# Kernel tuning notes

Measured on AMD Instinct MI355X. Metric: run time of the kernel, lower is better.

The kernel has to match this reference:

```python
import jax, jax.numpy as jnp
import numpy as np

Z_DIM = 3
H = 128
N_BLOCKS = 4
N = 30000
E = 180000
T = 2


def _mlp2(x, W1, b1, W2, b2):
    return jnp.maximum(x @ W1 + b1, 0.0) @ W2 + b2


def _stats(x, eps=1e-8):
    # batch mean/std as accumulated by the running-stat Normalizer (buffers -> no grad)
    m = x.mean(0)
    v = jnp.maximum((x * x).mean(0) - m * m, 0.0)
    s = jnp.maximum(jnp.sqrt(v), eps)
    return jax.lax.stop_gradient(m), jax.lax.stop_gradient(s)


def setup_inputs() -> dict:
    key = jax.random.key(0)
    ks = jax.random.split(key, 32)

    def w(k, shape, fan_in):
        return jax.random.normal(k, shape, jnp.float32) / np.sqrt(fan_in).astype(np.float32)

    inp = {}
    inp["z"] = jax.random.normal(ks[0], (T, N, Z_DIM), jnp.float32)
    inp["z_target"] = jax.random.normal(ks[1], (N, Z_DIM), jnp.float32)
    inp["pos"] = jax.random.uniform(ks[2], (N, 2), jnp.float32)
    # encoder node MLP: z_dim -> H -> H
    inp["enc_node_W1"] = w(ks[3], (Z_DIM, H), Z_DIM)
    inp["enc_node_b1"] = jnp.zeros((H,), jnp.float32)
    inp["enc_node_W2"] = w(ks[4], (H, H), H)
    inp["enc_node_b2"] = jnp.zeros((H,), jnp.float32)
    # encoder edge MLP: edge_dim(3) -> H -> H
    inp["enc_edge_W1"] = w(ks[5], (3, H), 3)
    inp["enc_edge_b1"] = jnp.zeros((H,), jnp.float32)
    inp["enc_edge_W2"] = w(ks[6], (H, H), H)
    inp["enc_edge_b2"] = jnp.zeros((H,), jnp.float32)
    # decoder MLP: H -> H -> z_dim
    inp["dec_W1"] = w(ks[7], (H, H), H)
    inp["dec_b1"] = jnp.zeros((H,), jnp.float32)
    inp["dec_W2"] = w(ks[8], (H, Z_DIM), H)
    inp["dec_b2"] = jnp.zeros((Z_DIM,), jnp.float32)
    # GraphNetBlocks, stacked over n_blocks
    inp["blk_edge_W1"] = w(ks[9], (N_BLOCKS, 3 * H, H), 3 * H)
    inp["blk_edge_b1"] = jnp.zeros((N_BLOCKS, H), jnp.float32)
    inp["blk_edge_W2"] = w(ks[10], (N_BLOCKS, H, H), H)
    inp["blk_edge_b2"] = jnp.zeros((N_BLOCKS, H), jnp.float32)
    inp["blk_node_W1"] = w(ks[11], (N_BLOCKS, 2 * H, H), 2 * H)
    inp["blk_node_b1"] = jnp.zeros((N_BLOCKS, H), jnp.float32)
    inp["blk_node_W2"] = w(ks[12], (N_BLOCKS, H, H), H)
    inp["blk_node_b2"] = jnp.zeros((N_BLOCKS, H), jnp.float32)
    # bidirectional mesh edges (triangles_to_edges output)
    inp["senders"] = jax.random.randint(ks[13], (E,), 0, N, jnp.int64)
    inp["receivers"] = jax.random.randint(ks[14], (E,), 0, N, jnp.int64)
    return inp


def reference(z, z_target, pos,
              enc_node_W1, enc_node_b1, enc_node_W2, enc_node_b2,
              enc_edge_W1, enc_edge_b1, enc_edge_W2, enc_edge_b2,
              dec_W1, dec_b1, dec_W2, dec_b2,
              blk_edge_W1, blk_edge_b1, blk_edge_W2, blk_edge_b2,
              blk_node_W1, blk_node_b1, blk_node_W2, blk_node_b2,
              senders, receivers):
    zl = z[-1]                                   # [N, z_dim]
    n_nodes = zl.shape[0]

    # --- build_graph ---
    rel = pos[senders] - pos[receivers]          # [E, 2]
    ef_raw = jnp.concatenate([rel, jnp.linalg.norm(rel, axis=1, keepdims=True)], axis=1)  # [E, 3]
    em, es = _stats(ef_raw)
    ef = _mlp2((ef_raw - em) / es, enc_edge_W1, enc_edge_b1, enc_edge_W2, enc_edge_b2)    # [E, H]
    nm, ns = _stats(zl)
    nf = _mlp2((zl - nm) / ns, enc_node_W1, enc_node_b1, enc_node_W2, enc_node_b2)        # [N, H]

    # --- message passing blocks ---
    def block(carry, p):
        nf, ef = carry
        eW1, eb1, eW2, eb2, nW1, nb1, nW2, nb2 = p
        e_in = jnp.concatenate([ef, nf[senders], nf[receivers]], axis=1)   # [E, 3H]
        ef = _mlp2(e_in, eW1, eb1, eW2, eb2) + ef
        agg = jax.ops.segment_sum(ef, receivers, num_segments=n_nodes)    # [N, H]
        n_in = jnp.concatenate([nf, agg], axis=1)                          # [N, 2H]
        nf = _mlp2(n_in, nW1, nb1, nW2, nb2) + nf
        return (nf, ef), None

    (nf, ef), _ = jax.lax.scan(block, (nf, ef),
                               (blk_edge_W1, blk_edge_b1, blk_edge_W2, blk_edge_b2,
                                blk_node_W1, blk_node_b1, blk_node_W2, blk_node_b2))

    # --- decode + loss ---
    output = _mlp2(nf, dec_W1, dec_b1, dec_W2, dec_b2)                     # [N, z_dim]
    target = z_target - zl
    om, os = _stats(target)
    target_normalized = (target - om) / os
    loss = jnp.mean((target_normalized - output) ** 2)

    z_update = jax.lax.stop_gradient(output) * os + om                     # Normalizer.inverse(detach)
    z_pred = zl + z_update
    rmse = jnp.mean(jnp.sqrt(jnp.mean((z_pred - z_target) ** 2, axis=0)))
    return z_pred, loss, rmse
```

## Files before the change

### kernel.cpp

```cpp
#include <hip/hip_runtime.h>
#include <hip/hip_bf16.h>
#include <math.h>

#define HDIM 128
#define TPB 256

typedef __attribute__((ext_vector_type(8))) short bf16x8;
typedef __attribute__((ext_vector_type(4))) float f32x4;

static inline int ceil_div(int a, int b){ return (a + b - 1) / b; }

__device__ __forceinline__ float wave_sum(float v){
#pragma unroll
  for (int o = 32; o > 0; o >>= 1) v += __shfl_down(v, o, 64);
  return v;
}

__device__ __forceinline__ short f2bf(float f){
  __hip_bfloat16 h = __float2bfloat16(f);
  return *reinterpret_cast<short*>(&h);
}
__device__ __forceinline__ float bfb2f(short s){
  unsigned int u = ((unsigned int)(unsigned short)s) << 16;
  return __builtin_bit_cast(float, u);
}

__device__ __forceinline__ void gl_lds16(const short* g, short* l){
  __builtin_amdgcn_global_load_lds(
      (const __attribute__((address_space(1))) void*)g,
      (__attribute__((address_space(3))) void*)l, 16, 0, 0);
}

__global__ void edge_raw_stats(const float* __restrict__ pos,
                               const int* __restrict__ snd,
                               const int* __restrict__ rcv,
                               float* __restrict__ ef_raw,
                               float* __restrict__ epart, int E){
  __shared__ float red[4][6];
  int tid = threadIdx.x, w = tid >> 6, l = tid & 63;
  int e = blockIdx.x * blockDim.x + tid;
  float s[6] = {0.f,0.f,0.f,0.f,0.f,0.f};
  if (e < E){
    int si = snd[e], ri = rcv[e];
    float rx = pos[2*si]   - pos[2*ri];
    float ry = pos[2*si+1] - pos[2*ri+1];
    float nm = sqrtf(rx*rx + ry*ry);
    ef_raw[3*e]   = rx;
    ef_raw[3*e+1] = ry;
    ef_raw[3*e+2] = nm;
    s[0] = rx; s[1] = ry; s[2] = nm;
    s[3] = rx*rx; s[4] = ry*ry; s[5] = nm*nm;
  }
#pragma unroll
  for (int k = 0; k < 6; k++) s[k] = wave_sum(s[k]);
  if (l == 0)
#pragma unroll
    for (int k = 0; k < 6; k++) red[w][k] = s[k];
  __syncthreads();
  if (tid < 6)
    epart[(size_t)blockIdx.x * 6 + tid] =
      red[0][tid] + red[1][tid] + red[2][tid] + red[3][tid];
}

__global__ void node_stats(const float* __restrict__ zl,
                           const float* __restrict__ z_target,
                           float* __restrict__ npart, int N){
  __shared__ float red[4][12];
  int tid = threadIdx.x, w = tid >> 6, l = tid & 63;
  int n = blockIdx.x * blockDim.x + tid;
  float s[12];
#pragma unroll
  for (int i = 0; i < 12; i++) s[i] = 0.f;
  if (n < N){
#pragma unroll
    for (int d = 0; d < 3; d++){
      float z = zl[3*n+d];
      float t = z_target[3*n+d] - z;
      s[d]   = z;  s[3+d] = z*z;
      s[6+d] = t;  s[9+d] = t*t;
    }
  }
#pragma unroll
  for (int i = 0; i < 12; i++) s[i] = wave_sum(s[i]);
  if (l == 0)
#pragma unroll
    for (int i = 0; i < 12; i++) red[w][i] = s[i];
  __syncthreads();
  if (tid < 12)
    npart[(size_t)blockIdx.x * 12 + tid] =
      red[0][tid] + red[1][tid] + red[2][tid] + red[3][tid];
}

__global__ void reduce_stats(const float* __restrict__ ep, int ne,
                             const float* __restrict__ np_, int nn,
                             float* __restrict__ raw){
  __shared__ float red[4];
  int tid = threadIdx.x, w = tid >> 6, l = tid & 63;
  for (int j = 0; j < 6; j++){
    float s = 0.f;
    for (int b = tid; b < ne; b += 256) s += ep[(size_t)b * 6 + j];
    s = wave_sum(s);
    if (l == 0) red[w] = s;
    __syncthreads();
    if (tid == 0) raw[j] = red[0] + red[1] + red[2] + red[3];
    __syncthreads();
  }
  for (int j = 0; j < 12; j++){
    float s = 0.f;
    for (int b = tid; b < nn; b += 256) s += np_[(size_t)b * 12 + j];
    s = wave_sum(s);
    if (l == 0) red[w] = s;
    __syncthreads();
    if (tid == 0) raw[6 + j] = red[0] + red[1] + red[2] + red[3];
    __syncthreads();
  }
}

__global__ void finalize_stats(const float* __restrict__ raw,
                               float* __restrict__ fin, int E, int N){
#pragma unroll
  for (int d = 0; d < 3; d++){
    float cE = (float)E, cN = (float)N;
    float m, v;
    m = raw[0+d] / cE; v = fmaxf(raw[3+d]/cE - m*m, 0.f);
    fin[0+d] = m;  fin[3+d]  = fmaxf(sqrtf(v), 1e-8f);
    m = raw[6+d] / cN; v = fmaxf(raw[9+d]/cN - m*m, 0.f);
    fin[6+d] = m;  fin[9+d]  = fmaxf(sqrtf(v), 1e-8f);
    m = raw[12+d] / cN; v = fmaxf(raw[15+d]/cN - m*m, 0.f);
    fin[12+d] = m; fin[15+d] = fmaxf(sqrtf(v), 1e-8f);
  }
}

__global__ void csr_hist(const int* __restrict__ rcv, int* __restrict__ deg, int E){
  int e = blockIdx.x * blockDim.x + threadIdx.x;
  if (e < E) atomicAdd(&deg[rcv[e]], 1);
}

__global__ void csr_scan(const int* __restrict__ deg, int* __restrict__ row_start,
                         int N, int E){
  __shared__ int part[1024];
  int t = threadIdx.x;
  int chunk = (N + 1023) / 1024;
  int lo = t * chunk, hi = min(lo + chunk, N);
  int s = 0;
  for (int i = lo; i < hi; i++) s += deg[i];
  part[t] = s;
  __syncthreads();
  for (int off = 1; off < 1024; off <<= 1){
    int v = (t >= off) ? part[t - off] : 0;
    __syncthreads();
    part[t] += v;
    __syncthreads();
  }
  int base = (t == 0) ? 0 : part[t - 1];
  for (int i = lo; i < hi; i++){
    row_start[i] = base;
    base += deg[i];
  }
  if (t == 1023) row_start[N] = E;
}

__global__ void csr_scatter(const int* __restrict__ rcv, int* __restrict__ cursor,
                            int* __restrict__ eids, int E){
  int e = blockIdx.x * blockDim.x + threadIdx.x;
  if (e < E){
    int p = atomicAdd(&cursor[rcv[e]], 1);
    eids[p] = e;
  }
}

__global__ void pack_weights(const float* __restrict__ encEW2,
                             const float* __restrict__ encNW2,
                             const float* __restrict__ decW1,
                             const float* __restrict__ beW1,
                             const float* __restrict__ beW2,
                             const float* __restrict__ bnW1,
                             const float* __restrict__ bnW2,
                             __hip_bfloat16* __restrict__ wp){
  int y = blockIdx.y;
  const float* src; __hip_bfloat16* dst; int K;
  if (y == 0){ src = encEW2; dst = wp;          K = 128; }
  else if (y == 1){ src = encNW2; dst = wp + 16384; K = 128; }
  else if (y == 2){ src = decW1;  dst = wp + 32768; K = 128; }
  else {
    int b = (y - 3) >> 2, j = (y - 3) & 3;
    __hip_bfloat16* base = wp + 49152 + b * 114688;
    if (j == 0){ src = beW1 + b*49152; dst = base;          K = 384; }
    else if (j == 1){ src = beW2 + b*16384; dst = base + 49152; K = 128; }
    else if (j == 2){ src = bnW1 + b*32768; dst = base + 65536; K = 256; }
    else { src = bnW2 + b*16384; dst = base + 98304; K = 128; }
  }
  int id = blockIdx.x * blockDim.x + threadIdx.x;
  if (id >= 128 * K) return;
  int c = id >> 12;
  int r = id & 4095;
  int t = r >> 9;
  int l = (r >> 3) & 63;
  int j = r & 7;
  int k = c * 32 + ((l >> 4) << 3) + j;
  int n = t * 16 + (l & 15);
  dst[id] = __float2bfloat16(src[k * 128 + n]);
}

__launch_bounds__(256)
__global__ void encoder_fused(const float* __restrict__ raw,
                              const float* __restrict__ mptr,
                              const float* __restrict__ sptr,
                              const float* __restrict__ W1,
                              const float* __restrict__ b1,
                              const __hip_bfloat16* __restrict__ W2f,
                              const float* __restrict__ b2,
                              __hip_bfloat16* __restrict__ out, int rows){
  __shared__ __align__(16) short bsh[16384];
  const int tid = threadIdx.x, w = tid >> 6, l = tid & 63, m = l & 15, q = l >> 4;
  const short* wsrc = (const short*)W2f;
#pragma unroll
  for (int i = 0; i < 8; i++){
    int inst = w * 8 + i;
    gl_lds16(wsrc + inst * 512 + l * 8, &bsh[inst * 512]);
  }

  float s0 = mptr[0], s1 = mptr[1], s2 = mptr[2];
  float d0 = sptr[0], d1 = sptr[1], d2 = sptr[2];
  const int row0 = blockIdx.x * 64 + w * 16;
  const int ra = min(row0 + m, rows - 1);
  float x0 = (raw[3*ra]   - s0) / d0;
  float x1 = (raw[3*ra+1] - s1) / d1;
  float x2 = (raw[3*ra+2] - s2) / d2;
  bf16x8 afr[4];
#pragma unroll
  for (int c = 0; c < 4; c++){
    int nb = c * 32 + q * 8;
#pragma unroll
    for (int j = 0; j < 8; j++){
      float h = b1[nb+j] + x0 * W1[nb+j] + x1 * W1[128+nb+j] + x2 * W1[256+nb+j];
      afr[c][j] = f2bf(fmaxf(h, 0.f));
    }
  }
  f32x4 acc[8];
#pragma unroll
  for (int t = 0; t < 8; t++) acc[t] = (f32x4){0.f,0.f,0.f,0.f};
  __syncthreads();
#pragma unroll
  for (int c = 0; c < 4; c++){
#pragma unroll
    for (int t = 0; t < 8; t++){
      bf16x8 b = *(const bf16x8*)&bsh[(c*8 + t)*512 + l*8];
      acc[t] = __builtin_amdgcn_mfma_f32_16x16x32_bf16(afr[c], b, acc[t], 0, 0, 0);
    }
  }
  const int row_d = row0 + q * 4;
#pragma unroll
  for (int t = 0; t < 8; t++){
    int col = t * 16 + m;
    float bb = b2[col];
#pragma unroll
    for (int r = 0; r < 4; r++){
      int e = row_d + r;
      if (e < rows) out[(size_t)e * HDIM + col] = __float2bfloat16(acc[t][r] + bb);
    }
  }
}

__launch_bounds__(256)
__global__ void gemm128_g(const __hip_bfloat16* __restrict__ A,
                          const __hip_bfloat16* __restrict__ Wf,
                          const float* __restrict__ bias,
                          float* __restrict__ out, int rows){
  __shared__ __align__(16) short bsh[16384];
  const int tid = threadIdx.x, w = tid >> 6, l = tid & 63, m = l & 15, q = l >> 4;
  const short* wsrc = (const short*)Wf;
#pragma unroll
  for (int i = 0; i < 8; i++){
    int inst = w * 8 + i;
    gl_lds16(wsrc + inst * 512 + l * 8, &bsh[inst * 512]);
  }
  const int row0 = blockIdx.x * 64 + w * 16;
  const int ra = min(row0 + m, rows - 1);
  const short* pa = (const short*)A + (size_t)ra * HDIM + q * 8;
  bf16x8 afr[4];
#pragma unroll
  for (int c = 0; c < 4; c++) afr[c] = *(const bf16x8*)(pa + c * 32);
  f32x4 acc[8];
#pragma unroll
  for (int t = 0; t < 8; t++) acc[t] = (f32x4){0.f,0.f,0.f,0.f};
  __syncthreads();
#pragma unroll
  for (int c = 0; c < 4; c++){
#pragma unroll
    for (int t = 0; t < 8; t++){
      bf16x8 b = *(const bf16x8*)&bsh[(c*8 + t)*512 + l*8];
      acc[t] = __builtin_amdgcn_mfma_f32_16x16x32_bf16(afr[c], b, acc[t], 0, 0, 0);
    }
  }
  const int row_d = row0 + q * 4;
#pragma unroll
  for (int t = 0; t < 8; t++){
    int col = t * 16 + m;
    float bb = bias[col];
#pragma unroll
    for (int r = 0; r < 4; r++){
      int e = row_d + r;
      if (e < rows) out[(size_t)e * HDIM + col] = fmaxf(acc[t][r] + bb, 0.f);
    }
  }
}

__launch_bounds__(256)
__global__ void edge_block(const int* __restrict__ snd,
                           const int* __restrict__ rcv,
                           const __hip_bfloat16* __restrict__ nf,
                           __hip_bfloat16* __restrict__ ef,
                           const __hip_bfloat16* __restrict__ Wfrag,
                           const float* __restrict__ b1,
                           const float* __restrict__ b2,
                           int E){
  __shared__ __align__(16) short bsh[2][4096];
  __shared__ __align__(16) short hsh[4][16][136];
  const int tid = threadIdx.x, w = tid >> 6, l = tid & 63, m = l & 15, q = l >> 4;
  const short* wsrc = (const short*)Wfrag;
  gl_lds16(wsrc + (w*2+0)*512 + l*8, &bsh[0][(w*2+0)*512]);
  gl_lds16(wsrc + (w*2+1)*512 + l*8, &bsh[0][(w*2+1)*512]);

  const int row0 = blockIdx.x * 64 + w * 16;
  const int ra = min(row0 + m, E - 1);
  const int si = snd[ra], ri = rcv[ra];
  const short* pe = (const short*)ef + (size_t)ra * HDIM + q * 8;
  const short* ps = (const short*)nf + (size_t)si * HDIM + q * 8;
  const short* pr = (const short*)nf + (size_t)ri * HDIM + q * 8;
  bf16x8 afr[12];
#pragma unroll
  for (int c = 0; c < 4; c++){
    afr[c]   = *(const bf16x8*)(pe + c * 32);
    afr[4+c] = *(const bf16x8*)(ps + c * 32);
    afr[8+c] = *(const bf16x8*)(pr + c * 32);
  }
  f32x4 acc[8];
#pragma unroll
  for (int t = 0; t < 8; t++) acc[t] = (f32x4){0.f,0.f,0.f,0.f};
  __syncthreads();
#pragma unroll
  for (int c = 0; c < 12; c++){
    {
      const short* src = wsrc + (c + 1) * 4096;
      short* dstb = &bsh[(c + 1) & 1][0];
      gl_lds16(src + (w*2+0)*512 + l*8, dstb + (w*2+0)*512);
      gl_lds16(src + (w*2+1)*512 + l*8, dstb + (w*2+1)*512);
    }
    const short* bb = &bsh[c & 1][0];
#pragma unroll
    for (int t = 0; t < 8; t++){
      bf16x8 b = *(const bf16x8*)(bb + t*512 + l*8);
      acc[t] = __builtin_amdgcn_mfma_f32_16x16x32_bf16(afr[c], b, acc[t], 0, 0, 0);
    }
    __syncthreads();
  }
#pragma unroll
  for (int t = 0; t < 8; t++){
    float bb = b1[t * 16 + m];
#pragma unroll
    for (int r = 0; r < 4; r++)
      hsh[w][q*4 + r][t*16 + m] = f2bf(fmaxf(acc[t][r] + bb, 0.f));
  }
  const short* ph = &hsh[w][m][0] + q * 8;
  f32x4 acc2[8];
#pragma unroll
  for (int t = 0; t < 8; t++) acc2[t] = (f32x4){0.f,0.f,0.f,0.f};
#pragma unroll
  for (int c = 12; c < 16; c++){
    if (c + 1 < 16){
      const short* src = wsrc + (c + 1) * 4096;
      short* dstb = &bsh[(c + 1) & 1][0];
      gl_lds16(src + (w*2+0)*512 + l*8, dstb + (w*2+0)*512);
      gl_lds16(src + (w*2+1)*512 + l*8, dstb + (w*2+1)*512);
    }
    bf16x8 a = *(const bf16x8*)(ph + (c - 12) * 32);
    const short* bb = &bsh[c & 1][0];
#pragma unroll
    for (int t = 0; t < 8; t++){
      bf16x8 b = *(const bf16x8*)(bb + t*512 + l*8);
      acc2[t] = __builtin_amdgcn_mfma_f32_16x16x32_bf16(a, b, acc2[t], 0, 0, 0);
    }
    if (c < 15) __syncthreads();
  }
#pragma unroll
  for (int t = 0; t < 8; t++){
    float bb = b2[t * 16 + m];
#pragma unroll
    for (int r = 0; r < 4; r++)
      hsh[w][q*4 + r][t*16 + m] = f2bf(acc2[t][r] + bb);
  }
  int orow = row0 + (l >> 2);
  if (orow < E){
    const short* src = &hsh[w][l >> 2][(l & 3) * 32];
    short* dst = (short*)ef + (size_t)orow * HDIM + (l & 3) * 32;
#pragma unroll
    for (int k = 0; k < 4; k++){
      bf16x8 vnew = *(const bf16x8*)(src + k * 8);
      bf16x8 vold = *(const bf16x8*)(dst + k * 8);
      bf16x8 vo;
#pragma unroll
      for (int j = 0; j < 8; j++) vo[j] = f2bf(bfb2f(vnew[j]) + bfb2f(vold[j]));
      *(bf16x8*)(dst + k * 8) = vo;
    }
  }
}

__launch_bounds__(256)
__global__ void node_block(const int* __restrict__ row_start,
                           const int* __restrict__ eids,
                           const __hip_bfloat16* __restrict__ ef,
                           __hip_bfloat16* __restrict__ nf,
                           const __hip_bfloat16* __restrict__ Wfrag,
                           const float* __restrict__ b1,
                           const float* __restrict__ b2,
                           int N){
  __shared__ __align__(16) short bsh[2][4096];
  __shared__ __align__(16) short hsh[4][16][136];
  const int tid = threadIdx.x, w = tid >> 6, l = tid & 63, m = l & 15, q = l >> 4;
  const short* wsrc = (const short*)Wfrag;
  gl_lds16(wsrc + (w*2+0)*512 + l*8, &bsh[0][(w*2+0)*512]);
  gl_lds16(wsrc + (w*2+1)*512 + l*8, &bsh[0][(w*2+1)*512]);

  const int row0 = blockIdx.x * 64 + w * 16;
  const int ra = min(row0 + m, N - 1);
  const short* pn = (const short*)nf + (size_t)ra * HDIM + q * 8;
  bf16x8 afr[8];
#pragma unroll
  for (int c = 0; c < 4; c++) afr[c] = *(const bf16x8*)(pn + c * 32);
  float sum[4][8];
#pragma unroll
  for (int c = 0; c < 4; c++)
#pragma unroll
    for (int j = 0; j < 8; j++) sum[c][j] = 0.f;
  int s0 = row_start[ra], s1 = row_start[ra + 1];
  for (int it = s0; it < s1; it++){
    int eid = eids[it];
    const short* pf = (const short*)ef + (size_t)eid * HDIM + q * 8;
#pragma unroll
    for (int c = 0; c < 4; c++){
      bf16x8 v = *(const bf16x8*)(pf + c * 32);
#pragma unroll
      for (int j = 0; j < 8; j++) sum[c][j] += bfb2f(v[j]);
    }
  }
#pragma unroll
  for (int c = 0; c < 4; c++)
#pragma unroll
    for (int j = 0; j < 8; j++) afr[4 + c][j] = f2bf(sum[c][j]);

  f32x4 acc[8];
#pragma unroll
  for (int t = 0; t < 8; t++) acc[t] = (f32x4){0.f,0.f,0.f,0.f};
  __syncthreads();
#pragma unroll
  for (int c = 0; c < 8; c++){
    {
      const short* src = wsrc + (c + 1) * 4096;
      short* dstb = &bsh[(c + 1) & 1][0];
      gl_lds16(src + (w*2+0)*512 + l*8, dstb + (w*2+0)*512);
      gl_lds16(src + (w*2+1)*512 + l*8, dstb + (w*2+1)*512);
    }
    const short* bb = &bsh[c & 1][0];
#pragma unroll
    for (int t = 0; t < 8; t++){
      bf16x8 b = *(const bf16x8*)(bb + t*512 + l*8);
      acc[t] = __builtin_amdgcn_mfma_f32_16x16x32_bf16(afr[c], b, acc[t], 0, 0, 0);
    }
    __syncthreads();
  }
#pragma unroll
  for (int t = 0; t < 8; t++){
    float bb = b1[t * 16 + m];
#pragma unroll
    for (int r = 0; r < 4; r++)
      hsh[w][q*4 + r][t*16 + m] = f2bf(fmaxf(acc[t][r] + bb, 0.f));
  }
  const short* ph = &hsh[w][m][0] + q * 8;
  f32x4 acc2[8];
#pragma unroll
  for (int t = 0; t < 8; t++) acc2[t] = (f32x4){0.f,0.f,0.f,0.f};
#pragma unroll
  for (int c = 8; c < 12; c++){
    if (c + 1 < 12){
      const short* src = wsrc + (c + 1) * 4096;
      short* dstb = &bsh[(c + 1) & 1][0];
      gl_lds16(src + (w*2+0)*512 + l*8, dstb + (w*2+0)*512);
      gl_lds16(src + (w*2+1)*512 + l*8, dstb + (w*2+1)*512);
    }
    bf16x8 a = *(const bf16x8*)(ph + (c - 8) * 32);
    const short* bb = &bsh[c & 1][0];
#pragma unroll
    for (int t = 0; t < 8; t++){
      bf16x8 b = *(const bf16x8*)(bb + t*512 + l*8);
      acc2[t] = __builtin_amdgcn_mfma_f32_16x16x32_bf16(a, b, acc2[t], 0, 0, 0);
    }
    if (c < 11) __syncthreads();
  }
#pragma unroll
  for (int t = 0; t < 8; t++){
    float bb = b2[t * 16 + m];
#pragma unroll
    for (int r = 0; r < 4; r++)
      hsh[w][q*4 + r][t*16 + m] = f2bf(acc2[t][r] + bb);
  }
  int orow = row0 + (l >> 2);
  if (orow < N){
    const short* src = &hsh[w][l >> 2][(l & 3) * 32];
    short* dst = (short*)nf + (size_t)orow * HDIM + (l & 3) * 32;
#pragma unroll
    for (int k = 0; k < 4; k++){
      bf16x8 vnew = *(const bf16x8*)(src + k * 8);
      bf16x8 vold = *(const bf16x8*)(dst + k * 8);
      bf16x8 vo;
#pragma unroll
      for (int j = 0; j < 8; j++) vo[j] = f2bf(bfb2f(vnew[j]) + bfb2f(vold[j]));
      *(bf16x8*)(dst + k * 8) = vo;
    }
  }
}

__global__ void dec_final(const float* __restrict__ hbuf,
                          const float* __restrict__ W2,
                          const float* __restrict__ b2,
                          float* __restrict__ outd, int rows){
  __shared__ float hl[64 * 129];
  __shared__ float Wl[HDIM * 3];
  __shared__ float bl[3];
  int t = threadIdx.x;
  int node0 = blockIdx.x * 64;
  for (int i = t; i < HDIM * 3; i += 256) Wl[i] = W2[i];
  if (t < 3) bl[t] = b2[t];
#pragma unroll
  for (int i = 0; i < 32; i++){
    int lin = t + i * 256;
    int r = lin >> 7;
    int c = lin & 127;
    int node = node0 + r;
    hl[r * 129 + c] = (node < rows) ? hbuf[(size_t)node * HDIM + c] : 0.f;
  }
  __syncthreads();
  if (t < 64){
    int node = node0 + t;
    if (node < rows){
      float a0 = bl[0], a1 = bl[1], a2 = bl[2];
      for (int k = 0; k < HDIM; k++){
        float v = hl[t * 129 + k];
        a0 += v * Wl[k * 3];
        a1 += v * Wl[k * 3 + 1];
        a2 += v * Wl[k * 3 + 2];
      }
      outd[3 * node]     = a0;
      outd[3 * node + 1] = a1;
      outd[3 * node + 2] = a2;
    }
  }
}

__global__ void epilogue(const float* __restrict__ dec_out,
                         const float* __restrict__ zl,
                         const float* __restrict__ z_target,
                         const float* __restrict__ fin,
                         float* __restrict__ d_out,
                         float* __restrict__ lpart, int N){
  __shared__ float red[4][4];
  int tid = threadIdx.x, w = tid >> 6, l = tid & 63;
  int n = blockIdx.x * blockDim.x + tid;
  float s[4] = {0.f,0.f,0.f,0.f};
  if (n < N){
#pragma unroll
    for (int d = 0; d < 3; d++){
      float om = fin[12 + d], os = fin[15 + d];
      float o   = dec_out[3*n + d];
      float zld = zl[3*n + d];
      float zt  = z_target[3*n + d];
      float tgt = zt - zld;
      float tn  = (tgt - om) / os;
      float diff = tn - o;
      s[0] += diff * diff;
      float zp = zld + o * os + om;
      d_out[3*n + d] = zp;
      float e = zp - zt;
      s[1 + d] = e * e;
    }
  }
#pragma unroll
  for (int k = 0; k < 4; k++) s[k] = wave_sum(s[k]);
  if (l == 0)
#pragma unroll
    for (int k = 0; k < 4; k++) red[w][k] = s[k];
  __syncthreads();
  if (tid < 4)
    lpart[(size_t)blockIdx.x * 4 + tid] =
      red[0][tid] + red[1][tid] + red[2][tid] + red[3][tid];
}

__global__ void finalize_out(const float* __restrict__ lpart, int nb,
                             float* __restrict__ d_out, int N){
  __shared__ float red[4];
  __shared__ float vals[4];
  int tid = threadIdx.x, w = tid >> 6, l = tid & 63;
  for (int j = 0; j < 4; j++){
    float s = 0.f;
    for (int b = tid; b < nb; b += 256) s += lpart[(size_t)b * 4 + j];
    s = wave_sum(s);
    if (l == 0) red[w] = s;
    __syncthreads();
    if (tid == 0) vals[j] = red[0] + red[1] + red[2] + red[3];
    __syncthreads();
  }
  if (tid == 0){
    float cN = (float)N;
    float loss = vals[0] / (3.f * cN);
    float rmse = (sqrtf(vals[1] / cN) + sqrtf(vals[2] / cN) + sqrtf(vals[3] / cN)) / 3.f;
    d_out[(size_t)3 * N]     = loss;
    d_out[(size_t)3 * N + 1] = rmse;
  }
}

extern "C" void kernel_launch(void* const* d_in, const int* in_sizes, int n_in,
                              void* d_out, int out_size, void* d_ws, size_t ws_size,
                              hipStream_t stream){
  const float* z           = (const float*)d_in[0];
  const float* z_target    = (const float*)d_in[1];
  const float* pos         = (const float*)d_in[2];
  const float* enc_node_W1 = (const float*)d_in[3];
  const float* enc_node_b1 = (const float*)d_in[4];
  const float* enc_node_W2 = (const float*)d_in[5];
  const float* enc_node_b2 = (const float*)d_in[6];
  const float* enc_edge_W1 = (const float*)d_in[7];
  const float* enc_edge_b1 = (const float*)d_in[8];
  const float* enc_edge_W2 = (const float*)d_in[9];
  const float* enc_edge_b2 = (const float*)d_in[10];
  const float* dec_W1      = (const float*)d_in[11];
  const float* dec_b1      = (const float*)d_in[12];
  const float* dec_W2      = (const float*)d_in[13];
  const float* dec_b2      = (const float*)d_in[14];
  const float* blk_edge_W1 = (const float*)d_in[15];
  const float* blk_edge_b1 = (const float*)d_in[16];
  const float* blk_edge_W2 = (const float*)d_in[17];
  const float* blk_edge_b2 = (const float*)d_in[18];
  const float* blk_node_W1 = (const float*)d_in[19];
  const float* blk_node_b1 = (const float*)d_in[20];
  const float* blk_node_W2 = (const float*)d_in[21];
  const float* blk_node_b2 = (const float*)d_in[22];
  const int*   senders     = (const int*)d_in[23];
  const int*   receivers   = (const int*)d_in[24];

  const int N = in_sizes[1] / 3;
  const int E = in_sizes[23];
  const float* zl = z + (size_t)N * 3;

  const int neb = ceil_div(E, TPB);
  const int nnb = ceil_div(N, TPB);

  char* p = (char*)d_ws;
  auto carve = [&](size_t bytes) -> char* {
    char* r = p; p += (bytes + 255) & ~(size_t)255; return r;
  };
  float* stats_raw = (float*)carve(32 * 4);
  float* stats_fin = (float*)carve(32 * 4);
  float* epart     = (float*)carve((size_t)neb * 6 * 4);
  float* npart     = (float*)carve((size_t)nnb * 12 * 4);
  float* lpart     = (float*)carve((size_t)nnb * 4 * 4);
  float* ef_raw    = (float*)carve((size_t)E * 3 * 4);
  float* dec_out   = (float*)carve((size_t)N * 3 * 4);
  float* hbuf      = (float*)carve((size_t)N * HDIM * 4);
  int*   deg       = (int*)carve((size_t)N * 4);
  int*   row_start = (int*)carve((size_t)(N + 1) * 4);
  int*   cursor    = (int*)carve((size_t)N * 4);
  int*   eids      = (int*)carve((size_t)E * 4);
  __hip_bfloat16* wp = (__hip_bfloat16*)carve((size_t)507904 * 2);
  __hip_bfloat16* ef = (__hip_bfloat16*)carve((size_t)E * HDIM * 2);
  __hip_bfloat16* nf = (__hip_bfloat16*)carve((size_t)N * HDIM * 2);

  float* out = (float*)d_out;

  hipMemsetAsync(deg, 0, (size_t)N * 4, stream);

  edge_raw_stats<<<neb, TPB, 0, stream>>>(pos, senders, receivers, ef_raw, epart, E);
  node_stats<<<nnb, TPB, 0, stream>>>(zl, z_target, npart, N);
  reduce_stats<<<1, TPB, 0, stream>>>(epart, neb, npart, nnb, stats_raw);
  finalize_stats<<<1, 1, 0, stream>>>(stats_raw, stats_fin, E, N);

  csr_hist<<<neb, TPB, 0, stream>>>(receivers, deg, E);
  csr_scan<<<1, 1024, 0, stream>>>(deg, row_start, N, E);
  hipMemcpyAsync(cursor, row_start, (size_t)N * 4, hipMemcpyDeviceToDevice, stream);
  csr_scatter<<<neb, TPB, 0, stream>>>(receivers, cursor, eids, E);

  pack_weights<<<dim3(192, 19), TPB, 0, stream>>>(enc_edge_W2, enc_node_W2, dec_W1,
                                                  blk_edge_W1, blk_edge_W2,
                                                  blk_node_W1, blk_node_W2, wp);

  encoder_fused<<<ceil_div(E, 64), TPB, 0, stream>>>(ef_raw, stats_fin + 0, stats_fin + 3,
                                                     enc_edge_W1, enc_edge_b1,
                                                     wp, enc_edge_b2, ef, E);
  encoder_fused<<<ceil_div(N, 64), TPB, 0, stream>>>(zl, stats_fin + 6, stats_fin + 9,
                                                     enc_node_W1, enc_node_b1,
                                                     wp + 16384, enc_node_b2, nf, N);

  for (int b = 0; b < 4; b++){
    const __hip_bfloat16* eWf = wp + 49152 + (size_t)b * 114688;
    const __hip_bfloat16* nWf = eWf + 65536;
    const float* eb1 = blk_edge_b1 + (size_t)b * 128;
    const float* eb2 = blk_edge_b2 + (size_t)b * 128;
    const float* nb1 = blk_node_b1 + (size_t)b * 128;
    const float* nb2 = blk_node_b2 + (size_t)b * 128;

    edge_block<<<ceil_div(E, 64), TPB, 0, stream>>>(senders, receivers, nf, ef,
                                                    eWf, eb1, eb2, E);
    node_block<<<ceil_div(N, 64), TPB, 0, stream>>>(row_start, eids, ef, nf,
                                                    nWf, nb1, nb2, N);
  }

  gemm128_g<<<ceil_div(N, 64), TPB, 0, stream>>>(nf, wp + 32768, dec_b1, hbuf, N);
  dec_final<<<ceil_div(N, 64), TPB, 0, stream>>>(hbuf, dec_W2, dec_b2, dec_out, N);

  epilogue<<<nnb, TPB, 0, stream>>>(dec_out, zl, z_target, stats_fin,
                                    out, lpart, N);
  finalize_out<<<1, TPB, 0, stream>>>(lpart, nnb, out, N);
}
```

Baseline: 602.7 us.

## Store edges in receiver-sorted order and use 512-thread blocks for GNN blocks

Builds the CSR before the edge encoder and permutes edge features into receiver-sorted order, so the node aggregation reads contiguous edge rows instead of going through an eids indirection. The edge and receiver gathers in the edge kernel also become more local because edges sharing a receiver sit next to each other. Separately, edge_block and node_block now run 8 waves over 128 rows per block, so each wave loads one weight fragment per stage instead of two. This adds sorted sender and receiver arrays and doubles the LDS used for hidden staging.

```diff
diff --git a/kernel.cpp b/kernel.cpp
--- a/kernel.cpp
+++ b/kernel.cpp
@@ -31,9 +31,55 @@
       (__attribute__((address_space(3))) void*)l, 16, 0, 0);
 }
 
+__global__ void csr_hist(const int* __restrict__ rcv, int* __restrict__ deg, int E){
+  int e = blockIdx.x * blockDim.x + threadIdx.x;
+  if (e < E) atomicAdd(&deg[rcv[e]], 1);
+}
+
+__global__ void csr_scan(const int* __restrict__ deg, int* __restrict__ row_start,
+                         int N, int E){
+  __shared__ int part[1024];
+  int t = threadIdx.x;
+  int chunk = (N + 1023) / 1024;
+  int lo = t * chunk, hi = min(lo + chunk, N);
+  int s = 0;
+  for (int i = lo; i < hi; i++) s += deg[i];
+  part[t] = s;
+  __syncthreads();
+  for (int off = 1; off < 1024; off <<= 1){
+    int v = (t >= off) ? part[t - off] : 0;
+    __syncthreads();
+    part[t] += v;
+    __syncthreads();
+  }
+  int base = (t == 0) ? 0 : part[t - 1];
+  for (int i = lo; i < hi; i++){
+    row_start[i] = base;
+    base += deg[i];
+  }
+  if (t == 1023) row_start[N] = E;
+}
+
+__global__ void csr_scatter(const int* __restrict__ snd,
+                            const int* __restrict__ rcv,
+                            int* __restrict__ cursor,
+                            int* __restrict__ pinv,
+                            int* __restrict__ psnd,
+                            int* __restrict__ prcv, int E){
+  int e = blockIdx.x * blockDim.x + threadIdx.x;
+  if (e < E){
+    int r = rcv[e];
+    int p = atomicAdd(&cursor[r], 1);
+    pinv[e] = p;
+    psnd[p] = snd[e];
+    prcv[p] = r;
+  }
+}
+
 __global__ void edge_raw_stats(const float* __restrict__ pos,
                                const int* __restrict__ snd,
                                const int* __restrict__ rcv,
+                               const int* __restrict__ pinv,
                                float* __restrict__ ef_raw,
                                float* __restrict__ epart, int E){
   __shared__ float red[4][6];
@@ -45,9 +91,10 @@
     float rx = pos[2*si]   - pos[2*ri];
     float ry = pos[2*si+1] - pos[2*ri+1];
     float nm = sqrtf(rx*rx + ry*ry);
-    ef_raw[3*e]   = rx;
-    ef_raw[3*e+1] = ry;
-    ef_raw[3*e+2] = nm;
+    int p = pinv[e];
+    ef_raw[3*p]   = rx;
+    ef_raw[3*p+1] = ry;
+    ef_raw[3*p+2] = nm;
     s[0] = rx; s[1] = ry; s[2] = nm;
     s[3] = rx*rx; s[4] = ry*ry; s[5] = nm*nm;
   }
@@ -128,44 +175,6 @@
     fin[6+d] = m;  fin[9+d]  = fmaxf(sqrtf(v), 1e-8f);
     m = raw[12+d] / cN; v = fmaxf(raw[15+d]/cN - m*m, 0.f);
     fin[12+d] = m; fin[15+d] = fmaxf(sqrtf(v), 1e-8f);
-  }
-}
-
-__global__ void csr_hist(const int* __restrict__ rcv, int* __restrict__ deg, int E){
-  int e = blockIdx.x * blockDim.x + threadIdx.x;
-  if (e < E) atomicAdd(&deg[rcv[e]], 1);
-}
-
-__global__ void csr_scan(const int* __restrict__ deg, int* __restrict__ row_start,
-                         int N, int E){
-  __shared__ int part[1024];
-  int t = threadIdx.x;
-  int chunk = (N + 1023) / 1024;
-  int lo = t * chunk, hi = min(lo + chunk, N);
-  int s = 0;
-  for (int i = lo; i < hi; i++) s += deg[i];
-  part[t] = s;
-  __syncthreads();
-  for (int off = 1; off < 1024; off <<= 1){
-    int v = (t >= off) ? part[t - off] : 0;
-    __syncthreads();
-    part[t] += v;
-    __syncthreads();
-  }
-  int base = (t == 0) ? 0 : part[t - 1];
-  for (int i = lo; i < hi; i++){
-    row_start[i] = base;
-    base += deg[i];
-  }
-  if (t == 1023) row_start[N] = E;
-}
-
-__global__ void csr_scatter(const int* __restrict__ rcv, int* __restrict__ cursor,
-                            int* __restrict__ eids, int E){
-  int e = blockIdx.x * blockDim.x + threadIdx.x;
-  if (e < E){
-    int p = atomicAdd(&cursor[rcv[e]], 1);
-    eids[p] = e;
   }
 }
 
@@ -219,7 +228,6 @@
     int inst = w * 8 + i;
     gl_lds16(wsrc + inst * 512 + l * 8, &bsh[inst * 512]);
   }
-
   float s0 = mptr[0], s1 = mptr[1], s2 = mptr[2];
   float d0 = sptr[0], d1 = sptr[1], d2 = sptr[2];
   const int row0 = blockIdx.x * 64 + w * 16;
@@ -306,9 +314,9 @@
   }
 }
 
-__launch_bounds__(256)
-__global__ void edge_block(const int* __restrict__ snd,
-                           const int* __restrict__ rcv,
+__launch_bounds__(512)
+__global__ void edge_block(const int* __restrict__ psnd,
+                           const int* __restrict__ prcv,
                            const __hip_bfloat16* __restrict__ nf,
                            __hip_bfloat16* __restrict__ ef,
                            const __hip_bfloat16* __restrict__ Wfrag,
@@ -316,15 +324,14 @@
                            const float* __restrict__ b2,
                            int E){
   __shared__ __align__(16) short bsh[2][4096];
-  __shared__ __align__(16) short hsh[4][16][136];
+  __shared__ __align__(16) short hsh[8][16][136];
   const int tid = threadIdx.x, w = tid >> 6, l = tid & 63, m = l & 15, q = l >> 4;
   const short* wsrc = (const short*)Wfrag;
-  gl_lds16(wsrc + (w*2+0)*512 + l*8, &bsh[0][(w*2+0)*512]);
-  gl_lds16(wsrc + (w*2+1)*512 + l*8, &bsh[0][(w*2+1)*512]);
-
-  const int row0 = blockIdx.x * 64 + w * 16;
+  gl_lds16(wsrc + w*512 + l*8, &bsh[0][w*512]);
+
+  const int row0 = blockIdx.x * 128 + w * 16;
   const int ra = min(row0 + m, E - 1);
-  const int si = snd[ra], ri = rcv[ra];
+  const int si = psnd[ra], ri = prcv[ra];
   const short* pe = (const short*)ef + (size_t)ra * HDIM + q * 8;
   const short* ps = (const short*)nf + (size_t)si * HDIM + q * 8;
   const short* pr = (const short*)nf + (size_t)ri * HDIM + q * 8;
@@ -341,12 +348,7 @@
   __syncthreads();
 #pragma unroll
   for (int c = 0; c < 12; c++){
-    {
-      const short* src = wsrc + (c + 1) * 4096;
-      short* dstb = &bsh[(c + 1) & 1][0];
-      gl_lds16(src + (w*2+0)*512 + l*8, dstb + (w*2+0)*512);
-      gl_lds16(src + (w*2+1)*512 + l*8, dstb + (w*2+1)*512);
-    }
+    gl_lds16(wsrc + (c+1)*4096 + w*512 + l*8, &bsh[(c+1)&1][w*512]);
     const short* bb = &bsh[c & 1][0];
 #pragma unroll
     for (int t = 0; t < 8; t++){
@@ -368,12 +370,8 @@
   for (int t = 0; t < 8; t++) acc2[t] = (f32x4){0.f,0.f,0.f,0.f};
 #pragma unroll
   for (int c = 12; c < 16; c++){
-    if (c + 1 < 16){
-      const short* src = wsrc + (c + 1) * 4096;
-      short* dstb = &bsh[(c + 1) & 1][0];
-      gl_lds16(src + (w*2+0)*512 + l*8, dstb + (w*2+0)*512);
-      gl_lds16(src + (w*2+1)*512 + l*8, dstb + (w*2+1)*512);
-    }
+    if (c + 1 < 16)
+      gl_lds16(wsrc + (c+1)*4096 + w*512 + l*8, &bsh[(c+1)&1][w*512]);
     bf16x8 a = *(const bf16x8*)(ph + (c - 12) * 32);
     const short* bb = &bsh[c & 1][0];
 #pragma unroll
@@ -406,9 +404,8 @@
   }
 }
 
-__launch_bounds__(256)
+__launch_bounds__(512)
 __global__ void node_block(const int* __restrict__ row_start,
-                           const int* __restrict__ eids,
                            const __hip_bfloat16* __restrict__ ef,
                            __hip_bfloat16* __restrict__ nf,
                            const __hip_bfloat16* __restrict__ Wfrag,
@@ -416,13 +413,12 @@
                            const float* __restrict__ b2,
                            int N){
   __shared__ __align__(16) short bsh[2][4096];
-  __shared__ __align__(16) short hsh[4][16][136];
+  __shared__ __align__(16) short hsh[8][16][136];
   const int tid = threadIdx.x, w = tid >> 6, l = tid & 63, m = l & 15, q = l >> 4;
   const short* wsrc = (const short*)Wfrag;
-  gl_lds16(wsrc + (w*2+0)*512 + l*8, &bsh[0][(w*2+0)*512]);
-  gl_lds16(wsrc + (w*2+1)*512 + l*8, &bsh[0][(w*2+1)*512]);
-
-  const int row0 = blockIdx.x * 64 + w * 16;
+  gl_lds16(wsrc + w*512 + l*8, &bsh[0][w*512]);
+
+  const int row0 = blockIdx.x * 128 + w * 16;
   const int ra = min(row0 + m, N - 1);
   const short* pn = (const short*)nf + (size_t)ra * HDIM + q * 8;
   bf16x8 afr[8];
@@ -435,8 +431,7 @@
     for (int j = 0; j < 8; j++) sum[c][j] = 0.f;
   int s0 = row_start[ra], s1 = row_start[ra + 1];
   for (int it = s0; it < s1; it++){
-    int eid = eids[it];
-    const short* pf = (const short*)ef + (size_t)eid * HDIM + q * 8;
+    const short* pf = (const short*)ef + (size_t)it * HDIM + q * 8;
 #pragma unroll
     for (int c = 0; c < 4; c++){
       bf16x8 v = *(const bf16x8*)(pf + c * 32);
@@ -455,12 +450,7 @@
   __syncthreads();
 #pragma unroll
   for (int c = 0; c < 8; c++){
-    {
-      const short* src = wsrc + (c + 1) * 4096;
-      short* dstb = &bsh[(c + 1) & 1][0];
-      gl_lds16(src + (w*2+0)*512 + l*8, dstb + (w*2+0)*512);
-      gl_lds16(src + (w*2+1)*512 + l*8, dstb + (w*2+1)*512);
-    }
+    gl_lds16(wsrc + (c+1)*4096 + w*512 + l*8, &bsh[(c+1)&1][w*512]);
     const short* bb = &bsh[c & 1][0];
 #pragma unroll
     for (int t = 0; t < 8; t++){
@@ -482,12 +472,8 @@
   for (int t = 0; t < 8; t++) acc2[t] = (f32x4){0.f,0.f,0.f,0.f};
 #pragma unroll
   for (int c = 8; c < 12; c++){
-    if (c + 1 < 12){
-      const short* src = wsrc + (c + 1) * 4096;
-      short* dstb = &bsh[(c + 1) & 1][0];
-      gl_lds16(src + (w*2+0)*512 + l*8, dstb + (w*2+0)*512);
-      gl_lds16(src + (w*2+1)*512 + l*8, dstb + (w*2+1)*512);
-    }
+    if (c + 1 < 12)
+      gl_lds16(wsrc + (c+1)*4096 + w*512 + l*8, &bsh[(c+1)&1][w*512]);
     bf16x8 a = *(const bf16x8*)(ph + (c - 8) * 32);
     const short* bb = &bsh[c & 1][0];
 #pragma unroll
@@ -669,7 +655,9 @@
   int*   deg       = (int*)carve((size_t)N * 4);
   int*   row_start = (int*)carve((size_t)(N + 1) * 4);
   int*   cursor    = (int*)carve((size_t)N * 4);
-  int*   eids      = (int*)carve((size_t)E * 4);
+  int*   pinv      = (int*)carve((size_t)E * 4);
+  int*   psnd      = (int*)carve((size_t)E * 4);
+  int*   prcv      = (int*)carve((size_t)E * 4);
   __hip_bfloat16* wp = (__hip_bfloat16*)carve((size_t)507904 * 2);
   __hip_bfloat16* ef = (__hip_bfloat16*)carve((size_t)E * HDIM * 2);
   __hip_bfloat16* nf = (__hip_bfloat16*)carve((size_t)N * HDIM * 2);
@@ -678,15 +666,15 @@
 
   hipMemsetAsync(deg, 0, (size_t)N * 4, stream);
 
-  edge_raw_stats<<<neb, TPB, 0, stream>>>(pos, senders, receivers, ef_raw, epart, E);
+  csr_hist<<<neb, TPB, 0, stream>>>(receivers, deg, E);
+  csr_scan<<<1, 1024, 0, stream>>>(deg, row_start, N, E);
+  hipMemcpyAsync(cursor, row_start, (size_t)N * 4, hipMemcpyDeviceToDevice, stream);
+  csr_scatter<<<neb, TPB, 0, stream>>>(senders, receivers, cursor, pinv, psnd, prcv, E);
+
+  edge_raw_stats<<<neb, TPB, 0, stream>>>(pos, senders, receivers, pinv, ef_raw, epart, E);
   node_stats<<<nnb, TPB, 0, stream>>>(zl, z_target, npart, N);
   reduce_stats<<<1, TPB, 0, stream>>>(epart, neb, npart, nnb, stats_raw);
   finalize_stats<<<1, 1, 0, stream>>>(stats_raw, stats_fin, E, N);
-
-  csr_hist<<<neb, TPB, 0, stream>>>(receivers, deg, E);
-  csr_scan<<<1, 1024, 0, stream>>>(deg, row_start, N, E);
-  hipMemcpyAsync(cursor, row_start, (size_t)N * 4, hipMemcpyDeviceToDevice, stream);
-  csr_scatter<<<neb, TPB, 0, stream>>>(receivers, cursor, eids, E);
 
   pack_weights<<<dim3(192, 19), TPB, 0, stream>>>(enc_edge_W2, enc_node_W2, dec_W1,
                                                   blk_edge_W1, blk_edge_W2,
@@ -707,10 +695,10 @@
     const float* nb1 = blk_node_b1 + (size_t)b * 128;
     const float* nb2 = blk_node_b2 + (size_t)b * 128;
 
-    edge_block<<<ceil_div(E, 64), TPB, 0, stream>>>(senders, receivers, nf, ef,
-                                                    eWf, eb1, eb2, E);
-    node_block<<<ceil_div(N, 64), TPB, 0, stream>>>(row_start, eids, ef, nf,
-                                                    nWf, nb1, nb2, N);
+    edge_block<<<ceil_div(E, 128), 512, 0, stream>>>(psnd, prcv, nf, ef,
+                                                     eWf, eb1, eb2, E);
+    node_block<<<ceil_div(N, 128), 512, 0, stream>>>(row_start, ef, nf,
+                                                     nWf, nb1, nb2, N);
   }
 
   gemm128_g<<<ceil_div(N, 64), TPB, 0, stream>>>(nf, wp + 32768, dec_b1, hbuf, N);
```

Measured after the change: 573.8 us. 4.8% less time.
